# Performance work log

Hardware: AMD Instinct MI355X
Metric: run time of the kernel (lower is better)

## Reference

```python
import jax, jax.numpy as jnp
import numpy as np

N_NODES = 50000
N_EDGES = 800000
H, D_IN, D_OUT = 4, 256, 64


def setup_inputs() -> dict:
    key = jax.random.key(0)
    ks = jax.random.split(key, 7)
    x = jax.random.normal(ks[0], (N_NODES, D_IN), dtype=jnp.float32)
    idx = jax.random.randint(ks[1], (2, N_EDGES), 0, N_NODES, dtype=jnp.int32)
    elem = jax.random.uniform(ks[2], (N_EDGES,), dtype=jnp.float32)
    Ws = jax.random.normal(ks[3], (H, D_IN, D_OUT), dtype=jnp.float32) * 0.05
    bs = jax.random.normal(ks[4], (H, D_OUT), dtype=jnp.float32) * 0.05
    aw = jax.random.normal(ks[5], (H, 2 * D_OUT + 1), dtype=jnp.float32) * 0.05
    ab = jax.random.normal(ks[6], (H,), dtype=jnp.float32) * 0.05
    return {"x": x, "idx": idx, "elem": elem, "Ws": Ws, "bs": bs, "aw": aw, "ab": ab}


def reference(x, idx, elem, Ws, bs, aw, ab):
    N = x.shape[0]
    O = Ws.shape[-1]
    # per-head MLP (num_mlp_layers=1 -> single Linear): [H, N, O]
    feats = jnp.einsum('nd,hdo->hno', x, Ws) + bs[:, None, :]
    # attention linear on concat(src, dst, elem): split weights instead of
    # materializing the [E, 2O+1] concat; math is identical.
    aw_src, aw_dst, aw_e = aw[:, :O], aw[:, O:2 * O], aw[:, 2 * O]
    a_s = jnp.einsum('hno,ho->hn', feats, aw_src)   # [H, N]
    a_d = jnp.einsum('hno,ho->hn', feats, aw_dst)   # [H, N]
    src, dst = idx[0], idx[1]
    score = a_s[:, src] + a_d[:, dst] + aw_e[:, None] * elem[None, :] + ab[:, None]
    w = jnp.exp(-jax.nn.relu(score / 20.0))        # [H, E], in (0, 1]
    dst_f = feats[:, dst]                          # [H, E, O] gather
    seg = lambda vals: jax.ops.segment_sum(vals, src, num_segments=N)
    pooled = jax.vmap(lambda wi, fi: seg(wi[:, None] * fi))(w, dst_f)  # [H, N, O]
    row_sum = jax.vmap(lambda wi: seg(wi))(w)                          # [H, N]
    out = pooled / row_sum[:, :, None]
    # concat heads along feature dim: [N, H*O]
    return jnp.transpose(out, (1, 0, 2)).reshape(N, H * O)
```

## Files before the change

kernel.cpp:

```cpp
#include <hip/hip_runtime.h>
#include <math.h>

constexpr int DIN = 256;
constexpr int H   = 4;
constexpr int O   = 64;
constexpr int HO  = H * O;
constexpr int AWS = 2 * O + 1;
constexpr int BSH = 5;
constexpr int BINW = 1 << BSH;
constexpr int CAP = 768;
constexpr int HEB = 4096;

typedef __bf16 bf16x8 __attribute__((ext_vector_type(8)));
typedef __bf16 bf16x4 __attribute__((ext_vector_type(4)));
typedef float  f32x4  __attribute__((ext_vector_type(4)));

__device__ __forceinline__ float bf2f(unsigned short u) {
    union { unsigned int i; float f; } c;
    c.i = ((unsigned int)u) << 16;
    return c.f;
}

__device__ __forceinline__ void local_scan(const int* __restrict__ bsum, int n,
                                           int* hs, int* wsum)
{
    int* woff = wsum + 4;
    const int t = threadIdx.x;
    const int lane = t & 63, w = t >> 6;
    const int i0 = t * 4;
    int4 v = make_int4(0, 0, 0, 0);
    if (i0 + 3 < n) v = *(const int4*)&bsum[i0];
    else {
        if (i0     < n) v.x = bsum[i0];
        if (i0 + 1 < n) v.y = bsum[i0 + 1];
        if (i0 + 2 < n) v.z = bsum[i0 + 2];
    }
    const int tot = v.x + v.y + v.z + v.w;
    int s = tot;
    #pragma unroll
    for (int off = 1; off < 64; off <<= 1) {
        const int u = __shfl_up(s, off, 64);
        if (lane >= off) s += u;
    }
    if (lane == 63) wsum[w] = s;
    __syncthreads();
    if (t == 0) {
        int run = 0;
        #pragma unroll
        for (int j = 0; j < 4; ++j) { woff[j] = run; run += wsum[j]; }
    }
    __syncthreads();
    const int e0 = s - tot + woff[w];
    if (i0     < n) hs[i0]     = e0;
    if (i0 + 1 < n) hs[i0 + 1] = e0 + v.x;
    if (i0 + 2 < n) hs[i0 + 2] = e0 + v.x + v.y;
    if (i0 + 3 < n) hs[i0 + 3] = e0 + v.x + v.y + v.z;
    __syncthreads();
}

__global__ __launch_bounds__(256) void k_prep_hist(const float* __restrict__ Ws,
    __bf16* __restrict__ Bt, const int* __restrict__ idx, int E,
    int* __restrict__ rank, int* __restrict__ hist, int NB, int NBIN)
{
    __shared__ int lhist[2048];
    const int b = blockIdx.x, t = threadIdx.x;

    if (b < 256) {
        const int i = b * 256 + t;
        const int k = i & 255;
        const int n = i >> 8;
        Bt[n * 256 + k] = (__bf16)Ws[(n >> 6) * (DIN * O) + k * O + (n & 63)];
        return;
    }

    const int bh = b - 256;
    for (int k = t; k < NBIN; k += 256) lhist[k] = 0;
    __syncthreads();
    const int base_e = bh * HEB + t;
    #pragma unroll
    for (int i = 0; i < HEB / 256; ++i) {
        const int e = base_e + i * 256;
        if (e < E) rank[e] = atomicAdd(&lhist[idx[e] >> BSH], 1);
    }
    __syncthreads();
    for (int k = t; k < NBIN; k += 256)
        hist[(size_t)k * NB + bh] = lhist[k];
}

__global__ __launch_bounds__(256) void k_gemm_scan(const float* __restrict__ x,
    const __bf16* __restrict__ Bt, const float* __restrict__ bs,
    const float* __restrict__ aw, int N, int GB,
    __bf16* __restrict__ F, float* __restrict__ a_sT, float* __restrict__ a_dT,
    int* __restrict__ hist, int* __restrict__ bsum, int T)
{
    __shared__ union SM {
        __bf16 As[64][DIN + 8];
        int    scr[8];
    } sm;
    const int b = blockIdx.x;
    const int t = threadIdx.x;

    if (b >= GB) {
        const int bsc = b - GB;
        int* wsum = sm.scr;
        int* woff = wsum + 4;
        const int lane = t & 63, w = t >> 6;
        const int i0 = bsc * 1024 + t * 4;
        int4 v = make_int4(0, 0, 0, 0);
        if (i0 + 3 < T) v = *(const int4*)&hist[i0];
        else {
            if (i0     < T) v.x = hist[i0];
            if (i0 + 1 < T) v.y = hist[i0 + 1];
            if (i0 + 2 < T) v.z = hist[i0 + 2];
        }
        const int tot = v.x + v.y + v.z + v.w;
        int s = tot;
        #pragma unroll
        for (int off = 1; off < 64; off <<= 1) {
            const int u = __shfl_up(s, off, 64);
            if (lane >= off) s += u;
        }
        if (lane == 63) wsum[w] = s;
        __syncthreads();
        if (t == 0) {
            int run = 0;
            #pragma unroll
            for (int j = 0; j < 4; ++j) { woff[j] = run; run += wsum[j]; }
            bsum[bsc] = run;
        }
        __syncthreads();
        const int e0 = s - tot + woff[w];
        int4 o;
        o.x = e0; o.y = e0 + v.x; o.z = o.y + v.y; o.w = o.z + v.z;
        if (i0 + 3 < T) *(int4*)&hist[i0] = o;
        else {
            if (i0     < T) hist[i0]     = o.x;
            if (i0 + 1 < T) hist[i0 + 1] = o.y;
            if (i0 + 2 < T) hist[i0 + 2] = o.z;
        }
        return;
    }

    const int w    = t >> 6;
    const int lane = t & 63;
    const int c15  = lane & 15;
    const int quad = lane >> 4;
    const int n0   = b * 64;

    #pragma unroll
    for (int i = 0; i < 16; ++i) {
        const int r   = i * 4 + w;
        const int row = n0 + r;
        float4 xv = make_float4(0.f, 0.f, 0.f, 0.f);
        if (row < N) xv = *(const float4*)&x[(size_t)row * DIN + lane * 4];
        bf16x4 pv = { (__bf16)xv.x, (__bf16)xv.y, (__bf16)xv.z, (__bf16)xv.w };
        *(bf16x4*)&sm.As[r][lane * 4] = pv;
    }
    __syncthreads();

    f32x4 acc[4][4] = {};
    const __bf16* BtW = Bt + (size_t)(w * 64) * 256;
    const int kq = quad * 8;

    #pragma unroll
    for (int k0 = 0; k0 < DIN; k0 += 32) {
        bf16x8 afr[4], bfr[4];
        #pragma unroll
        for (int rt = 0; rt < 4; ++rt)
            afr[rt] = *(const bf16x8*)&sm.As[rt * 16 + c15][k0 + kq];
        #pragma unroll
        for (int ct = 0; ct < 4; ++ct)
            bfr[ct] = *(const bf16x8*)&BtW[(size_t)(ct * 16 + c15) * 256 + k0 + kq];
        #pragma unroll
        for (int rt = 0; rt < 4; ++rt)
            #pragma unroll
            for (int ct = 0; ct < 4; ++ct)
                acc[rt][ct] = __builtin_amdgcn_mfma_f32_16x16x32_bf16(
                    afr[rt], bfr[ct], acc[rt][ct], 0, 0, 0);
    }

    float bsv[4], awsv[4], awdv[4];
    #pragma unroll
    for (int ct = 0; ct < 4; ++ct) {
        const int col = ct * 16 + c15;
        bsv[ct]  = bs[w * 64 + col];
        awsv[ct] = aw[w * AWS + col];
        awdv[ct] = aw[w * AWS + O + col];
    }

    #pragma unroll
    for (int rt = 0; rt < 4; ++rt) {
        float psum[4] = {0.f, 0.f, 0.f, 0.f};
        float pdum[4] = {0.f, 0.f, 0.f, 0.f};
        #pragma unroll
        for (int ct = 0; ct < 4; ++ct) {
            #pragma unroll
            for (int reg = 0; reg < 4; ++reg) {
                const float f = acc[rt][ct][reg] + bsv[ct];
                const int row = n0 + rt * 16 + quad * 4 + reg;
                if (row < N)
                    F[(size_t)row * HO + w * 64 + ct * 16 + c15] = (__bf16)f;
                psum[reg] = fmaf(f, awsv[ct], psum[reg]);
                pdum[reg] = fmaf(f, awdv[ct], pdum[reg]);
            }
        }
        #pragma unroll
        for (int reg = 0; reg < 4; ++reg) {
            float v = psum[reg], u = pdum[reg];
            #pragma unroll
            for (int off = 1; off < 16; off <<= 1) {
                v += __shfl_xor(v, off, 64);
                u += __shfl_xor(u, off, 64);
            }
            const int row = n0 + rt * 16 + quad * 4 + reg;
            if (c15 == 0 && row < N) {
                a_sT[row * H + w] = v;
                a_dT[row * H + w] = u;
            }
        }
    }
}

__global__ __launch_bounds__(256) void k_scatter(const int* __restrict__ idx,
    const float* __restrict__ elem, const int* __restrict__ rank,
    const int* __restrict__ hist, const int* __restrict__ bsum, int nb1,
    int NB, int E, int2* __restrict__ csr)
{
    __shared__ int hs[1024];
    __shared__ int wsc[8];
    local_scan(bsum, nb1, hs, wsc);

    const int e = blockIdx.x * 256 + threadIdx.x;
    if (e >= E) return;
    const int s = idx[e];
    const int d = idx[E + e];
    const int i = (s >> BSH) * NB + (e / HEB);
    const int pos = hist[i] + hs[i >> 10] + rank[e];
    csr[pos] = make_int2((int)(((unsigned)s << 16) | (unsigned)d),
                         __float_as_int(elem[e]));
}

__global__ __launch_bounds__(256) void k_bingather(const int* __restrict__ hist,
    const int* __restrict__ bsum, int nb1, int NB, int NBIN, int N, int E,
    const float* __restrict__ a_sT, const float* __restrict__ a_dT,
    const float* __restrict__ aw, const float* __restrict__ ab,
    const int2* __restrict__ csr, const __bf16* __restrict__ F,
    float* __restrict__ out)
{
    __shared__ int hs[1024];
    __shared__ int wsc[8];
    __shared__ unsigned short ld[CAP];
    __shared__ float4 lw[CAP];
    __shared__ float4 s_as[BINW];
    __shared__ int h[BINW], cur[BINW], off_a[BINW + 1];

    local_scan(bsum, nb1, hs, wsc);

    const int k = blockIdx.x;
    const int t = threadIdx.x;
    const int wv = t >> 6, lane = t & 63;

    const int i0 = k * NB;
    const int S = hist[i0] + hs[i0 >> 10];
    int Snext = E;
    if (k + 1 < NBIN) {
        const int i1 = (k + 1) * NB;
        Snext = hist[i1] + hs[i1 >> 10];
    }
    int cnt = Snext - S;
    if (cnt > CAP) cnt = CAP;

    if (t < BINW) {
        h[t] = 0;
        const int node = k * BINW + t;
        s_as[t] = (node < N) ? *(const float4*)&a_sT[node * 4]
                             : make_float4(0.f, 0.f, 0.f, 0.f);
    }
    __syncthreads();

    for (int j = t; j < cnt; j += 256)
        atomicAdd(&h[((unsigned)csr[S + j].x >> 16) & (BINW - 1)], 1);
    __syncthreads();

    if (t < BINW) {
        const int v = h[t];
        int s = v;
        #pragma unroll
        for (int off = 1; off < BINW; off <<= 1) {
            const int u = __shfl_up(s, off, 64);
            if (t >= off) s += u;
        }
        const int excl = s - v;
        cur[t]   = excl;
        off_a[t] = excl;
        if (t == BINW - 1) off_a[BINW] = excl + v;
    }
    __syncthreads();

    const float4 ab4 = *(const float4*)&ab[0];
    const float4 awe4 = make_float4(aw[0 * AWS + 2 * O], aw[1 * AWS + 2 * O],
                                    aw[2 * AWS + 2 * O], aw[3 * AWS + 2 * O]);
    for (int j = t; j < cnt; j += 256) {
        const int2 r = csr[S + j];
        const unsigned sd = (unsigned)r.x;
        const int sl = (sd >> 16) & (BINW - 1);
        const int d  = (int)(sd & 0xFFFFu);
        const int pos = atomicAdd(&cur[sl], 1);
        const float el = __int_as_float(r.y);
        const float4 as = s_as[sl];
        const float4 ad = *(const float4*)&a_dT[d * 4];
        float4 w4;
        w4.x = __expf(-fmaxf((as.x + ad.x + awe4.x * el + ab4.x) * 0.05f, 0.f));
        w4.y = __expf(-fmaxf((as.y + ad.y + awe4.y * el + ab4.y) * 0.05f, 0.f));
        w4.z = __expf(-fmaxf((as.z + ad.z + awe4.z * el + ab4.z) * 0.05f, 0.f));
        w4.w = __expf(-fmaxf((as.w + ad.w + awe4.w * el + ab4.w) * 0.05f, 0.f));
        ld[pos] = (unsigned short)d;
        lw[pos] = w4;
    }
    __syncthreads();

    const int h16 = lane >> 4;
    const __bf16* __restrict__ Fl = F + lane * 4;
    const float* lwf = (const float*)&lw[0];

    for (int i = 0; i < BINW / 4; ++i) {
        const int nl = wv * (BINW / 4) + i;
        const int n  = k * BINW + nl;
        if (n >= N) continue;
        const int jb = off_a[nl];
        const int je = off_a[nl + 1];

        float4 acc = make_float4(0.f, 0.f, 0.f, 0.f);
        float  rs  = 0.f;
        int j = jb;
        for (; j + 8 <= je; j += 8) {
            int dd[8]; float ww[8]; ushort4 ff[8];
            #pragma unroll
            for (int q = 0; q < 8; ++q) {
                dd[q] = ld[j + q];
                ww[q] = lwf[(j + q) * 4 + h16];
            }
            #pragma unroll
            for (int q = 0; q < 8; ++q)
                ff[q] = *(const ushort4*)&Fl[(size_t)dd[q] * HO];
            #pragma unroll
            for (int q = 0; q < 8; ++q) {
                acc.x = fmaf(ww[q], bf2f(ff[q].x), acc.x);
                acc.y = fmaf(ww[q], bf2f(ff[q].y), acc.y);
                acc.z = fmaf(ww[q], bf2f(ff[q].z), acc.z);
                acc.w = fmaf(ww[q], bf2f(ff[q].w), acc.w);
                rs += ww[q];
            }
        }
        for (; j + 4 <= je; j += 4) {
            int dd[4]; float ww[4]; ushort4 ff[4];
            #pragma unroll
            for (int q = 0; q < 4; ++q) {
                dd[q] = ld[j + q];
                ww[q] = lwf[(j + q) * 4 + h16];
            }
            #pragma unroll
            for (int q = 0; q < 4; ++q)
                ff[q] = *(const ushort4*)&Fl[(size_t)dd[q] * HO];
            #pragma unroll
            for (int q = 0; q < 4; ++q) {
                acc.x = fmaf(ww[q], bf2f(ff[q].x), acc.x);
                acc.y = fmaf(ww[q], bf2f(ff[q].y), acc.y);
                acc.z = fmaf(ww[q], bf2f(ff[q].z), acc.z);
                acc.w = fmaf(ww[q], bf2f(ff[q].w), acc.w);
                rs += ww[q];
            }
        }
        for (; j < je; ++j) {
            const int d = ld[j];
            const float w = lwf[j * 4 + h16];
            const ushort4 fv = *(const ushort4*)&Fl[(size_t)d * HO];
            acc.x = fmaf(w, bf2f(fv.x), acc.x);
            acc.y = fmaf(w, bf2f(fv.y), acc.y);
            acc.z = fmaf(w, bf2f(fv.z), acc.z);
            acc.w = fmaf(w, bf2f(fv.w), acc.w);
            rs += w;
        }

        const float inv = 1.f / rs;
        float4 o = make_float4(acc.x * inv, acc.y * inv,
                               acc.z * inv, acc.w * inv);
        *(float4*)&out[(size_t)n * HO + lane * 4] = o;
    }
}

extern "C" void kernel_launch(void* const* d_in, const int* in_sizes, int n_in,
                              void* d_out, int out_size, void* d_ws, size_t ws_size,
                              hipStream_t stream)
{
    const float* x    = (const float*)d_in[0];
    const int*   idx  = (const int*)d_in[1];
    const float* elem = (const float*)d_in[2];
    const float* Ws   = (const float*)d_in[3];
    const float* bs   = (const float*)d_in[4];
    const float* aw   = (const float*)d_in[5];
    const float* ab   = (const float*)d_in[6];

    const int N    = in_sizes[0] / DIN;
    const int E    = in_sizes[1] / 2;
    const int GB   = (N + 63) / 64;
    const int NB   = (E + HEB - 1) / HEB;
    const int NBIN = (N + BINW - 1) / BINW;
    const int T    = NBIN * NB;
    const int nb1  = (T + 1023) / 1024;

    __bf16* F      = (__bf16*)d_ws;
    float* a_sT    = (float*)(F + (size_t)N * HO);
    float* a_dT    = a_sT + (size_t)N * H;
    int*   hist    = (int*)(a_dT + (size_t)N * H);
    int*   bsum    = hist + ((T + 3) & ~3);
    int*   rank    = bsum + ((nb1 + 4) & ~3);
    size_t off = (size_t)((char*)(rank + E) - (char*)d_ws);
    off = (off + 15) & ~(size_t)15;
    int2*  csr     = (int2*)((char*)d_ws + off);
    __bf16* Bt     = (__bf16*)(csr + E);
    float* out     = (float*)d_out;

    k_prep_hist<<<256 + NB, 256, 0, stream>>>(Ws, Bt, idx, E, rank,
                                              hist, NB, NBIN);
    k_gemm_scan<<<GB + nb1, 256, 0, stream>>>(x, Bt, bs, aw, N, GB,
                                              F, a_sT, a_dT, hist, bsum, T);
    k_scatter<<<(E + 255) / 256, 256, 0, stream>>>(idx, elem, rank, hist,
                                                   bsum, nb1, NB, E, csr);
    k_bingather<<<NBIN, 256, 0, stream>>>(hist, bsum, nb1, NB, NBIN, N, E,
                                          a_sT, a_dT, aw, ab, csr, F, out);
}
```

Measured before the change: 236.5 us.

## Stage GEMM output through LDS for coalesced F stores; widen gather to 16B loads

The GEMM epilogue now writes bf16 features into shared memory and then stores full 512-byte rows to F with 16-byte coalesced stores, replacing scattered 2-byte stores. The aggregation kernel splits each wave into two halves that each process alternate edges with 16-byte (8 bf16) loads per lane, then combines the halves with a cross-lane shuffle. This targets memory transaction efficiency in both kernels. In exchange it adds two block barriers and reuses the As shared buffer, and it adds a shuffle reduction plus half-idle lanes during the output store.

```diff
diff --git a/kernel.cpp b/kernel.cpp
--- a/kernel.cpp
+++ b/kernel.cpp
@@ -19,6 +19,12 @@
     union { unsigned int i; float f; } c;
     c.i = ((unsigned int)u) << 16;
     return c.f;
+}
+__device__ __forceinline__ float bflo(unsigned u) {
+    union { unsigned i; float f; } c; c.i = u << 16; return c.f;
+}
+__device__ __forceinline__ float bfhi(unsigned u) {
+    union { unsigned i; float f; } c; c.i = u & 0xFFFF0000u; return c.f;
 }
 
 __device__ __forceinline__ void local_scan(const int* __restrict__ bsum, int n,
@@ -188,6 +194,8 @@
         awdv[ct] = aw[w * AWS + O + col];
     }
 
+    __syncthreads();
+
     #pragma unroll
     for (int rt = 0; rt < 4; ++rt) {
         float psum[4] = {0.f, 0.f, 0.f, 0.f};
@@ -197,9 +205,8 @@
             #pragma unroll
             for (int reg = 0; reg < 4; ++reg) {
                 const float f = acc[rt][ct][reg] + bsv[ct];
-                const int row = n0 + rt * 16 + quad * 4 + reg;
-                if (row < N)
-                    F[(size_t)row * HO + w * 64 + ct * 16 + c15] = (__bf16)f;
+                const int r = rt * 16 + quad * 4 + reg;
+                sm.As[r][w * 64 + ct * 16 + c15] = (__bf16)f;
                 psum[reg] = fmaf(f, awsv[ct], psum[reg]);
                 pdum[reg] = fmaf(f, awdv[ct], pdum[reg]);
             }
@@ -217,6 +224,18 @@
                 a_sT[row * H + w] = v;
                 a_dT[row * H + w] = u;
             }
+        }
+    }
+    __syncthreads();
+
+    const int sub = t & 31;
+    #pragma unroll
+    for (int q = 0; q < 8; ++q) {
+        const int r   = q * 8 + (t >> 5);
+        const int row = n0 + r;
+        if (row < N) {
+            const uint4 v = *(const uint4*)((const char*)&sm.As[r][0] + sub * 16);
+            *(uint4*)&F[(size_t)row * HO + sub * 8] = v;
         }
     }
 }
@@ -319,8 +338,10 @@
     }
     __syncthreads();
 
-    const int h16 = lane >> 4;
-    const __bf16* __restrict__ Fl = F + lane * 4;
+    const int half = lane >> 5;
+    const int sub  = lane & 31;
+    const int hh   = sub >> 3;
+    const __bf16* __restrict__ Fl = F + sub * 8;
     const float* lwf = (const float*)&lw[0];
 
     for (int i = 0; i < BINW / 4; ++i) {
@@ -330,62 +351,62 @@
         const int jb = off_a[nl];
         const int je = off_a[nl + 1];
 
-        float4 acc = make_float4(0.f, 0.f, 0.f, 0.f);
-        float  rs  = 0.f;
+        float acc[8] = {0.f, 0.f, 0.f, 0.f, 0.f, 0.f, 0.f, 0.f};
+        float rs = 0.f;
         int j = jb;
         for (; j + 8 <= je; j += 8) {
-            int dd[8]; float ww[8]; ushort4 ff[8];
-            #pragma unroll
-            for (int q = 0; q < 8; ++q) {
-                dd[q] = ld[j + q];
-                ww[q] = lwf[(j + q) * 4 + h16];
+            uint4 fv[4]; float ww[4];
+            #pragma unroll
+            for (int p = 0; p < 4; ++p) {
+                const int jj = j + p * 2 + half;
+                const int d  = ld[jj];
+                ww[p] = lwf[jj * 4 + hh];
+                fv[p] = *(const uint4*)&Fl[(size_t)d * HO];
             }
             #pragma unroll
-            for (int q = 0; q < 8; ++q)
-                ff[q] = *(const ushort4*)&Fl[(size_t)dd[q] * HO];
-            #pragma unroll
-            for (int q = 0; q < 8; ++q) {
-                acc.x = fmaf(ww[q], bf2f(ff[q].x), acc.x);
-                acc.y = fmaf(ww[q], bf2f(ff[q].y), acc.y);
-                acc.z = fmaf(ww[q], bf2f(ff[q].z), acc.z);
-                acc.w = fmaf(ww[q], bf2f(ff[q].w), acc.w);
-                rs += ww[q];
+            for (int p = 0; p < 4; ++p) {
+                acc[0] = fmaf(ww[p], bflo(fv[p].x), acc[0]);
+                acc[1] = fmaf(ww[p], bfhi(fv[p].x), acc[1]);
+                acc[2] = fmaf(ww[p], bflo(fv[p].y), acc[2]);
+                acc[3] = fmaf(ww[p], bfhi(fv[p].y), acc[3]);
+                acc[4] = fmaf(ww[p], bflo(fv[p].z), acc[4]);
+                acc[5] = fmaf(ww[p], bfhi(fv[p].z), acc[5]);
+                acc[6] = fmaf(ww[p], bflo(fv[p].w), acc[6]);
+                acc[7] = fmaf(ww[p], bfhi(fv[p].w), acc[7]);
+                rs += ww[p];
             }
         }
-        for (; j + 4 <= je; j += 4) {
-            int dd[4]; float ww[4]; ushort4 ff[4];
-            #pragma unroll
-            for (int q = 0; q < 4; ++q) {
-                dd[q] = ld[j + q];
-                ww[q] = lwf[(j + q) * 4 + h16];
-            }
-            #pragma unroll
-            for (int q = 0; q < 4; ++q)
-                ff[q] = *(const ushort4*)&Fl[(size_t)dd[q] * HO];
-            #pragma unroll
-            for (int q = 0; q < 4; ++q) {
-                acc.x = fmaf(ww[q], bf2f(ff[q].x), acc.x);
-                acc.y = fmaf(ww[q], bf2f(ff[q].y), acc.y);
-                acc.z = fmaf(ww[q], bf2f(ff[q].z), acc.z);
-                acc.w = fmaf(ww[q], bf2f(ff[q].w), acc.w);
-                rs += ww[q];
-            }
-        }
-        for (; j < je; ++j) {
-            const int d = ld[j];
-            const float w = lwf[j * 4 + h16];
-            const ushort4 fv = *(const ushort4*)&Fl[(size_t)d * HO];
-            acc.x = fmaf(w, bf2f(fv.x), acc.x);
-            acc.y = fmaf(w, bf2f(fv.y), acc.y);
-            acc.z = fmaf(w, bf2f(fv.z), acc.z);
-            acc.w = fmaf(w, bf2f(fv.w), acc.w);
-            rs += w;
-        }
+        for (; j < je; j += 2) {
+            const int jj = j + half;
+            int d; float w_;
+            if (jj < je) { d = ld[jj]; w_ = lwf[jj * 4 + hh]; }
+            else         { d = ld[j];  w_ = 0.f; }
+            const uint4 fv = *(const uint4*)&Fl[(size_t)d * HO];
+            acc[0] = fmaf(w_, bflo(fv.x), acc[0]);
+            acc[1] = fmaf(w_, bfhi(fv.x), acc[1]);
+            acc[2] = fmaf(w_, bflo(fv.y), acc[2]);
+            acc[3] = fmaf(w_, bfhi(fv.y), acc[3]);
+            acc[4] = fmaf(w_, bflo(fv.z), acc[4]);
+            acc[5] = fmaf(w_, bfhi(fv.z), acc[5]);
+            acc[6] = fmaf(w_, bflo(fv.w), acc[6]);
+            acc[7] = fmaf(w_, bfhi(fv.w), acc[7]);
+            rs += w_;
+        }
+
+        #pragma unroll
+        for (int q = 0; q < 8; ++q) acc[q] += __shfl_xor(acc[q], 32, 64);
+        rs += __shfl_xor(rs, 32, 64);
 
         const float inv = 1.f / rs;
-        float4 o = make_float4(acc.x * inv, acc.y * inv,
-                               acc.z * inv, acc.w * inv);
-        *(float4*)&out[(size_t)n * HO + lane * 4] = o;
+        if (half == 0) {
+            float* dst = &out[(size_t)n * HO + sub * 8];
+            float4 o0 = make_float4(acc[0] * inv, acc[1] * inv,
+                                    acc[2] * inv, acc[3] * inv);
+            float4 o1 = make_float4(acc[4] * inv, acc[5] * inv,
+                                    acc[6] * inv, acc[7] * inv);
+            *(float4*)dst       = o0;
+            *(float4*)(dst + 4) = o1;
+        }
     }
 }
 
```

New measurement: 230.4 us. -2.6%, faster.
